# Kernel tuning notes

Hardware: AMD Instinct MI355X
Metric: run time of the kernel (lower is better)

Reference implementation:

```python
import jax, jax.numpy as jnp
import numpy as np
from jax import lax

B, T_IN, N, C_IN = 64, 12, 716, 2
RC = DC = 32      # residual / dilation channels
SC = 8            # skip channels
EC = 512          # end channels
OUT = 12
DIMS = 40
DAYS = 288
TOD = 288
TOPK = 100
DILS = [1, 2, 1, 2, 1, 2, 1, 2]  # blocks=4, layers=2
L = len(DILS)


def setup_inputs() -> dict:
    key = jax.random.key(0)
    ks = iter(jax.random.split(key, 64))
    n = lambda shape, s=0.1: jax.random.normal(next(ks), shape, jnp.float32) * s
    return dict(
        history_data=jax.random.uniform(next(ks), (B, T_IN, N, C_IN), jnp.float32),
        alpha=jnp.float32(-5.0),
        nodevec_p1=n((DAYS, DIMS), 1.0),
        nodevec_p2=n((N, DIMS), 1.0),
        nodevec_p3=n((N, DIMS), 1.0),
        nodevec_pk=n((DIMS, DIMS, DIMS), 1.0),
        pivweight=n((N, N), 1.0),
        start_W=n((RC, 1)), start_b=n((RC,)),
        starta_W=n((1, 1)), starta_b=n((1,)),
        filter_W=n((L, DC, RC, 1, 2)), filter_b=n((L, DC)),
        gate_W=n((L, DC, RC, 1, 2)), gate_b=n((L, DC)),
        skip_W=n((L, SC, DC)), skip_b=n((L, SC)),
        gconv_W=n((L, RC, 3 * DC)), gconv_b=n((L, RC)),
        pgconv_W=n((L, RC, 3 * RC)), pgconv_b=n((L, RC)),
        bn_gamma=jnp.ones((L, RC), jnp.float32),
        bn_beta=jnp.zeros((L, RC), jnp.float32),
        end1_W=n((EC, SC * 52)), end1_b=n((EC,)),
        end2_W=n((OUT, EC)), end2_b=n((OUT,)),
    )


def _conv1x1(x, W, b):  # x [B,C,N,T], W [O,C]
    return jnp.einsum('bcnt,oc->bont', x, W) + b[None, :, None, None]


def _gcn(x, A, W, b):
    # diffusion order 2 over one support; A [B,N,N] or [N,N]
    sub = 'bcvt,bwv->bcwt' if A.ndim == 3 else 'bcvt,wv->bcwt'
    x1 = jnp.einsum(sub, x, A)
    x2 = jnp.einsum(sub, x1, A)
    return _conv1x1(jnp.concatenate([x, x1, x2], axis=1), W, b)


def _forward(history_data, alpha, nodevec_p1, nodevec_p2, nodevec_p3, nodevec_pk,
             pivweight, start_W, start_b, starta_W, starta_b,
             filter_W, filter_b, gate_W, gate_b, skip_W, skip_b,
             gconv_W, gconv_b, pgconv_W, pgconv_b, bn_gamma, bn_beta,
             end1_W, end1_b, end2_W, end2_b):
    inputs = jnp.transpose(history_data[..., 0:1], (0, 3, 2, 1))  # [B,1,N,T]
    inputs = jnp.pad(inputs, ((0, 0), (0, 0), (0, 0), (1, 0)))    # T -> 13 = receptive field
    ind = (history_data[:, -1, 0, 1] * TOD).astype(jnp.int32) % DAYS

    x = _conv1x1(inputs, start_W, start_b)      # [B,RC,N,13]
    x_a = _conv1x1(inputs, starta_W, starta_b)  # [B,1,N,13]

    # dynamic adjacency (dgconstruct)
    adp = jnp.einsum('ai,ijk->ajk', nodevec_p1[ind], nodevec_pk)
    adp = jnp.einsum('bj,ajk->abk', nodevec_p2, adp)
    adp = jnp.einsum('ck,abk->abc', nodevec_p3, adp)
    adj = jax.nn.softmax(jax.nn.relu(adp), axis=2)  # [B,N,N]

    # pivotal adjacency (pivotalconstruct) with top-k node mask
    xs = x_a[:, 0].sum(0)                   # [N,T]
    y = xs.sum(1)[None, :]                  # [1,N]
    adjp = (xs[:, :-1] @ xs[:, 1:].T) / y   # [N,N]
    adjp = adjp * pivweight
    score = adjp.sum(0) + adjp.sum(1)
    _, idx = lax.top_k(score, TOPK)
    mask = jnp.zeros((N,), bool).at[idx].set(True)
    adj_p = jax.nn.softmax(jax.nn.relu(adjp * mask[:, None] * mask[None, :]), axis=1)  # [N,N]

    a_s = jax.nn.sigmoid(alpha)
    dn = ('NCHW', 'OIHW', 'NCHW')
    skip = None
    for i, d in enumerate(DILS):
        residual = x
        filt = jnp.tanh(
            lax.conv_general_dilated(residual, filter_W[i], (1, 1), 'VALID',
                                     rhs_dilation=(1, d), dimension_numbers=dn)
            + filter_b[i][None, :, None, None])
        gate = jax.nn.sigmoid(
            lax.conv_general_dilated(residual, gate_W[i], (1, 1), 'VALID',
                                     rhs_dilation=(1, d), dimension_numbers=dn)
            + gate_b[i][None, :, None, None])
        xg = _gcn(filt * gate, adj, gconv_W[i], gconv_b[i])  # [B,RC,N,T-d]
        # pgcn: diffusion on residual, then causal temporal crop by dilation
        xa = _gcn(residual, adj_p, pgconv_W[i], pgconv_b[i])[..., : residual.shape[3] - d]
        x = a_s * xa + (1.0 - a_s) * xg
        x = x + residual[..., -x.shape[3]:]
        s = _conv1x1(x, skip_W[i], skip_b[i])  # [B,SC,N,Ti]
        s = jnp.transpose(s, (0, 1, 3, 2)).reshape(s.shape[0], -1, s.shape[2], 1)  # [B,SC*Ti,N,1]
        skip = s if skip is None else jnp.concatenate([s, skip], axis=1)
        # BatchNorm2d, train-mode batch stats, fresh affine
        mu = x.mean(axis=(0, 2, 3), keepdims=True)
        var = x.var(axis=(0, 2, 3), keepdims=True)
        x = ((x - mu) / jnp.sqrt(var + 1e-5)) * bn_gamma[i][None, :, None, None] \
            + bn_beta[i][None, :, None, None]

    out = jax.nn.relu(skip)                         # [B,SC*52,N,1]
    out = jax.nn.relu(_conv1x1(out, end1_W, end1_b))
    out = _conv1x1(out, end2_W, end2_b)             # [B,OUT,N,1]
    return out


def reference(history_data, alpha, nodevec_p1, nodevec_p2, nodevec_p3, nodevec_pk,
              pivweight, start_W, start_b, starta_W, starta_b,
              filter_W, filter_b, gate_W, gate_b, skip_W, skip_b,
              gconv_W, gconv_b, pgconv_W, pgconv_b, bn_gamma, bn_beta,
              end1_W, end1_b, end2_W, end2_b):
    return _forward(history_data, alpha, nodevec_p1, nodevec_p2, nodevec_p3, nodevec_pk,
                    pivweight, start_W, start_b, starta_W, starta_b,
                    filter_W, filter_b, gate_W, gate_b, skip_W, skip_b,
                    gconv_W, gconv_b, pgconv_W, pgconv_b, bn_gamma, bn_beta,
                    end1_W, end1_b, end2_W, end2_b)
```

## Files before the change

### kernel.cpp

```cpp
#include <hip/hip_runtime.h>
#include <math.h>

#define NN 716
#define NSQ (716*716)
#define MAXG 9216
#define FPAD 70
typedef unsigned short bfu;
typedef __attribute__((ext_vector_type(8))) __bf16 bf16x8;
typedef __attribute__((ext_vector_type(4))) float f32x4;

__device__ __forceinline__ float b2f(bfu u){ union{unsigned int i; float f;} x; x.i = ((unsigned int)u)<<16; return x.f; }
__device__ __forceinline__ bfu f2b(float f){ union{float fv; unsigned int i;} x; x.fv = f; unsigned int r = (x.i + 0x7fffu + ((x.i>>16)&1u)) >> 16; return (bfu)r; }
__device__ __forceinline__ float sigmoidf_(float x){ return 1.f/(1.f+expf(-x)); }

__device__ __forceinline__ float fexp_(float x){
#if __has_builtin(__builtin_amdgcn_exp2f)
  return __builtin_amdgcn_exp2f(x * 1.44269504088896340736f);
#else
  return __expf(x);
#endif
}
__device__ __forceinline__ float frcp_(float x){
#if __has_builtin(__builtin_amdgcn_rcpf)
  return __builtin_amdgcn_rcpf(x);
#else
  return 1.f/x;
#endif
}
__device__ __forceinline__ float fsig_(float x){ return frcp_(1.f + fexp_(-x)); }
__device__ __forceinline__ float ftanh_(float x){
  float xc = fminf(fmaxf(x, -30.f), 30.f);
  float e = fexp_(-2.f*xc);
  return (1.f - e) * frcp_(1.f + e);
}


__global__ void k_ind(const float* __restrict__ hist, int* __restrict__ ind){
  int b = threadIdx.x; if (b >= 64) return;
  float v = hist[((b*12+11)*NN + 0)*2 + 1];
  ind[b] = ((int)(v*288.0f)) % 288;
}

__global__ void k_dg1(const float* __restrict__ p1, const float* __restrict__ pk,
                      const int* __restrict__ ind, float* __restrict__ tmp1){
  int b = blockIdx.x;
  __shared__ float p1s[40];
  if (threadIdx.x < 40) p1s[threadIdx.x] = p1[ind[b]*40 + threadIdx.x];
  __syncthreads();
  for (int jk = threadIdx.x; jk < 1600; jk += 256){
    float acc = 0.f;
    for (int i = 0; i < 40; ++i) acc += p1s[i]*pk[i*1600 + jk];
    tmp1[b*1600 + jk] = acc;
  }
}

__global__ void k_dg2(const float* __restrict__ p2, const float* __restrict__ tmp1,
                      float* __restrict__ tmp2){
  int b = blockIdx.y;
  __shared__ float ts[1600];
  for (int i = threadIdx.x; i < 1600; i += 256) ts[i] = tmp1[b*1600+i];
  __syncthreads();
  int idx = blockIdx.x*256 + threadIdx.x;
  if (idx >= NN*40) return;
  int n = idx/40, k = idx%40;
  float acc = 0.f;
  for (int j = 0; j < 40; ++j) acc += p2[n*40+j]*ts[j*40+k];
  tmp2[(long)b*NN*40 + idx] = acc;
}

__global__ void k_p3t(const float* __restrict__ p3, float* __restrict__ p3t){
  int v = blockIdx.x*256 + threadIdx.x; if (v >= NN) return;
  for (int k = 0; k < 40; ++k) p3t[k*NN + v] = p3[v*40 + k];
}

__global__ __launch_bounds__(256) void k_adjrow4s(const float* __restrict__ p3t,
    const float* __restrict__ tmp2, unsigned int* __restrict__ topA,
    int* __restrict__ cntA)
{
  int b = blockIdx.y, w0 = blockIdx.x*4, tid = threadIdx.x;
  int wave = tid >> 6, lane = tid & 63;
  __shared__ float t2s[4][40];
  __shared__ float buf[4][720];
  __shared__ float wred[4][4];
  __shared__ float rstat[4];
  __shared__ int pc[4][12];
  for (int i = tid; i < 160; i += 256){
    int r = i/40, k = i%40; int w = w0 + r;
    t2s[r][k] = (w < NN) ? tmp2[((long)b*NN + w)*40 + k] : 0.f;
  }
  __syncthreads();
  float lmax[4] = {0,0,0,0};
  for (int q = 0; q < 3; ++q){
    int v = tid + q*256;
    if (v < NN){
      float a[4] = {0,0,0,0};
      #pragma unroll 8
      for (int k = 0; k < 40; ++k){
        float pv = p3t[k*NN + v];
        #pragma unroll
        for (int r = 0; r < 4; ++r) a[r] += t2s[r][k]*pv;
      }
      #pragma unroll
      for (int r = 0; r < 4; ++r){
        float val = fmaxf(a[r], 0.f);
        buf[r][v] = val;
        lmax[r] = fmaxf(lmax[r], val);
      }
    }
  }
  #pragma unroll
  for (int r = 0; r < 4; ++r){
    float m = lmax[r];
    for (int s = 32; s > 0; s >>= 1) m = fmaxf(m, __shfl_xor(m, s, 64));
    if (lane == 0) wred[r][wave] = m;
  }
  __syncthreads();
  if (tid < 4) rstat[tid] = fmaxf(fmaxf(wred[tid][0], wred[tid][1]), fmaxf(wred[tid][2], wred[tid][3]));
  __syncthreads();
  float lsum[4] = {0,0,0,0};
  for (int q = 0; q < 3; ++q){
    int v = tid + q*256;
    if (v < NN){
      #pragma unroll
      for (int r = 0; r < 4; ++r){
        float e = fexp_(buf[r][v] - rstat[r]);
        buf[r][v] = e;
        lsum[r] += e;
      }
    }
  }
  __syncthreads();
  #pragma unroll
  for (int r = 0; r < 4; ++r){
    float s = lsum[r];
    for (int k = 32; k > 0; k >>= 1) s += __shfl_xor(s, k, 64);
    if (lane == 0) wred[r][wave] = s;
  }
  __syncthreads();
  if (tid < 4) rstat[tid] = frcp_(wred[tid][0] + wred[tid][1] + wred[tid][2] + wred[tid][3]);
  __syncthreads();
  for (int q = 0; q < 3; ++q){
    int v = tid + q*256;
    #pragma unroll
    for (int r = 0; r < 4; ++r){
      float p = (v < NN) ? buf[r][v]*rstat[r] : 0.f;
      unsigned long long m = __ballot(p >= 1e-7f);
      if (lane == 0) pc[r][q*4+wave] = __popcll(m);
    }
  }
  __syncthreads();
  for (int q = 0; q < 3; ++q){
    int v = tid + q*256;
    #pragma unroll
    for (int r = 0; r < 4; ++r){
      float p = (v < NN) ? buf[r][v]*rstat[r] : 0.f;
      bool qual = (p >= 1e-7f);
      unsigned long long m = __ballot(qual);
      int w = w0 + r;
      if (qual && w < NN){
        int base = 0, me = q*4+wave;
        for (int s = 0; s < me; ++s) base += pc[r][s];
        unsigned long long below = (lane == 0) ? 0ull : (m << (64-lane) >> (64-lane));
        int pos = base + __popcll(below);
        if (pos < 16)
          topA[((long)b*NN + w)*16 + pos] = (((unsigned)v)<<16) | (unsigned)f2b(p);
      }
    }
  }
  __syncthreads();
  if (tid < 4){
    int w = w0 + tid;
    if (w < NN){
      int tot = 0;
      for (int s = 0; s < 12; ++s) tot += pc[tid][s];
      cntA[(long)b*NN + w] = (tot < 16) ? tot : 16;
    }
  }
}

__global__ __launch_bounds__(256) void k_zgather2(const bfu* __restrict__ Xg,
    const unsigned int* __restrict__ topA, const int* __restrict__ cntA,
    bfu* __restrict__ Z1g, bfu* __restrict__ Z2g, int M, long sx)
{
  __shared__ bfu rows[4][720];
  __shared__ bfu zrow[4][720];
  int b = blockIdx.y;
  int tid = threadIdx.x, wave = tid >> 6, lane = tid & 63;
  int m = blockIdx.x*4 + wave;
  if (m < M){
    const bfu* xr = Xg + (long)b*sx + (long)m*NN;
    #pragma unroll
    for (int q = 0; q < 12; ++q){
      int v = lane + q*64;
      if (v < NN) rows[wave][v] = xr[v];
    }
  }
  __syncthreads();
  const unsigned int* ta = topA + (long)b*NN*16;
  const int* ca = cntA + (long)b*NN;
  if (m < M){
    bfu* zr = Z1g + (long)b*sx + (long)m*NN;
    #pragma unroll
    for (int q = 0; q < 12; ++q){
      int w = lane + q*64;
      if (w < NN){
        int cnt = ca[w];
        const unsigned int* lst = ta + (long)w*16;
        float acc = 0.f;
        for (int j = 0; j < cnt; ++j){
          unsigned int e = lst[j];
          acc += b2f((bfu)(e & 0xffffu)) * b2f(rows[wave][e >> 16]);
        }
        bfu zv = f2b(acc);
        zr[w] = zv;
        zrow[wave][w] = zv;
      }
    }
  }
  __syncthreads();
  if (m >= M) return;
  bfu* z2r = Z2g + (long)b*sx + (long)m*NN;
  #pragma unroll
  for (int q = 0; q < 12; ++q){
    int w = lane + q*64;
    if (w < NN){
      int cnt = ca[w];
      const unsigned int* lst = ta + (long)w*16;
      float acc = 0.f;
      for (int j = 0; j < cnt; ++j){
        unsigned int e = lst[j];
        acc += b2f((bfu)(e & 0xffffu)) * b2f(zrow[wave][e >> 16]);
      }
      z2r[w] = f2b(acc);
    }
  }
}

__global__ void k_xs(const float* __restrict__ hist, const float* __restrict__ saW,
                     const float* __restrict__ sab, float* __restrict__ xs, float* __restrict__ y){
  int n = blockIdx.x, b = threadIdx.x;
  float w = saW[0], bb = sab[0];
  float ytot = 0.f;
  for (int t = 0; t < 13; ++t){
    float inp = (t == 0) ? 0.f : hist[((b*12 + (t-1))*NN + n)*2];
    float s = inp;
    for (int off = 32; off > 0; off >>= 1) s += __shfl_down(s, off, 64);
    if (b == 0){ float val = w*s + 64.f*bb; xs[n*13+t] = val; ytot += val; }
  }
  if (b == 0) y[n] = ytot;
}

__global__ void k_adjp(const float* __restrict__ xs, const float* __restrict__ y,
                       const float* __restrict__ piv, float* __restrict__ adjp){
  int i = blockIdx.y;
  __shared__ float xi[13];
  if (threadIdx.x < 13) xi[threadIdx.x] = xs[i*13+threadIdx.x];
  __syncthreads();
  int j = blockIdx.x*256 + threadIdx.x;
  if (j >= NN) return;
  float acc = 0.f;
  #pragma unroll
  for (int t = 0; t < 12; ++t) acc += xi[t]*xs[j*13+t+1];
  adjp[(long)i*NN+j] = acc / y[j] * piv[(long)i*NN+j];
}

__global__ void k_score(const float* __restrict__ adjp, float* __restrict__ score){
  int n = blockIdx.x, tid = threadIdx.x;
  float s = 0.f;
  for (int i = tid; i < NN; i += 256) s += adjp[(long)i*NN+n] + adjp[(long)n*NN+i];
  __shared__ float red[256];
  red[tid] = s; __syncthreads();
  for (int k = 128; k > 0; k >>= 1){ if (tid < k) red[tid] += red[tid+k]; __syncthreads(); }
  if (tid == 0) score[n] = red[0];
}

__global__ void k_topk(const float* __restrict__ score, int* __restrict__ mask){
  __shared__ float v[1024];
  __shared__ int ix[1024];
  int tid = threadIdx.x;
  for (int t = tid; t < 1024; t += 256){ v[t] = (t < NN) ? score[t] : -INFINITY; ix[t] = t; }
  __syncthreads();
  for (int k = 2; k <= 1024; k <<= 1){
    for (int j = k >> 1; j > 0; j >>= 1){
      for (int t = tid; t < 1024; t += 256){
        int l = t ^ j;
        if (l > t){
          bool up = ((t & k) == 0);
          bool g = (v[t] > v[l]) || (v[t] == v[l] && ix[t] < ix[l]);
          if (up ? !g : g){
            float tv = v[t]; v[t] = v[l]; v[l] = tv;
            int ti = ix[t]; ix[t] = ix[l]; ix[l] = ti;
          }
        }
      }
      __syncthreads();
    }
  }
  for (int t = tid; t < NN; t += 256) mask[t] = 0;
  __syncthreads();
  if (tid < 100) mask[ix[tid]] = 1;
}

__global__ void k_pivprep(const float* __restrict__ adjp, const int* __restrict__ mask,
                          int* __restrict__ idxk, int* __restrict__ rankv,
                          float* __restrict__ uvec, float* __restrict__ ApkT){
  __shared__ int sidx[100];
  int tid = threadIdx.x;
  if (tid == 0){
    int c = 0;
    for (int i = 0; i < NN; ++i){
      if (mask[i] && c < 100){ sidx[c] = i; idxk[c] = i; rankv[i] = c; ++c; }
      else rankv[i] = -1;
    }
  }
  __syncthreads();
  if (tid < 100){
    int i = sidx[tid];
    const float* row = adjp + (long)i*NN;
    float mx = 0.f;
    for (int k = 0; k < 100; ++k) mx = fmaxf(mx, row[sidx[k]]);
    float sum = 616.f * fexp_(-mx);
    for (int k = 0; k < 100; ++k) sum += fexp_(fmaxf(row[sidx[k]], 0.f) - mx);
    float inv = 1.f/sum;
    uvec[tid] = fexp_(-mx)*inv;
    for (int k = 0; k < 100; ++k)
      ApkT[k*100 + tid] = fexp_(fmaxf(row[sidx[k]], 0.f) - mx)*inv;
  }
}

__global__ void k_init_x(const float* __restrict__ hist, const float* __restrict__ sW,
                         const float* __restrict__ sb, bfu* __restrict__ x){
  int n = blockIdx.x*256 + threadIdx.x; if (n >= NN) return;
  int t = blockIdx.y, b = blockIdx.z;
  float inp = (t == 0) ? 0.f : hist[((b*12 + (t-1))*NN + n)*2];
  #pragma unroll
  for (int c = 0; c < 32; ++c)
    x[((long)(b*32+c)*13 + t)*NN + n] = f2b(sW[c]*inp + sb[c]);
}

__global__ void k_bnid(float* __restrict__ bnp){
  int c = threadIdx.x; if (c >= 32) return;
  bnp[c*2] = 1.f; bnp[c*2+1] = 0.f;
}

__global__ void k_bnfold(const float* __restrict__ fW, const float* __restrict__ fb,
                         const float* __restrict__ gW, const float* __restrict__ gb,
                         const float* __restrict__ bnp, bfu* __restrict__ Wcat,
                         float* __restrict__ bcat){
  int tid = threadIdx.x;
  for (int i = tid; i < 4096; i += 256){
    int row = i >> 6, k = i & 63;
    int o = row >> 1, isg = row & 1;
    int tap = k >> 5, c = k & 31;
    const float* W = isg ? gW : fW;
    Wcat[i] = f2b(W[(o*32+c)*2 + tap] * bnp[c*2]);
  }
  if (tid < 64){
    int o = tid >> 1, isg = tid & 1;
    const float* W = isg ? gW : fW;
    const float* B = isg ? gb : fb;
    float s = B[o];
    for (int c = 0; c < 32; ++c)
      s += (W[(o*32+c)*2] + W[(o*32+c)*2+1]) * bnp[c*2+1];
    bcat[tid] = s;
  }
}

__global__ void k_e1perm(const float* __restrict__ W, bfu* __restrict__ Wb){
  int i = blockIdx.x*256 + threadIdx.x;
  if (i >= 512*416) return;
  int e = i/416, kp = i%416;
  const int off2[9] = {0,96,176,248,304,352,384,408,416};
  const int soff[8] = {320,240,168,112,64,32,8,0};
  const int tpl[8]  = {12,10,9,7,6,4,3,1};
  int L = 0;
  #pragma unroll
  for (int q = 0; q < 8; ++q) if (kp >= off2[q+1]) L = q+1;
  int r = kp - off2[L]; int t = r>>3, sc = r&7;
  int k = soff[L] + sc*tpl[L] + t;
  Wb[e*416+kp] = f2b(W[e*416+k]);
}

#define LDST 44

__global__ __launch_bounds__(256) void gemm_mfma(const bfu* __restrict__ Xg,
    const bfu* __restrict__ Ag, bfu* __restrict__ Cg,
    int M, int K, long sx, long sa, long sc,
    const float* __restrict__ bias, int relu_out, int Trow, int Tcomp)
{
  int bx = gridDim.x, by = gridDim.y, nb = gridDim.z;
  int bX = blockIdx.x, bY = blockIdx.y, bZ = blockIdx.z;
  int bpb = bx*by, total = bpb*nb;
  if ((total & 7) == 0 && (nb & 7) == 0){
    int L = bX + bx*(bY + by*bZ);
    int xcd = L & 7, slot = L >> 3;
    bZ = xcd*(nb >> 3) + slot/bpb;
    int inner = slot % bpb;
    bX = inner % bx; bY = inner / bx;
  }
  const bfu* X = Xg + (long)bZ*sx;
  const bfu* A = Ag + (long)bZ*sa;
  bfu*       C = Cg + (long)bZ*sc;
  int m0 = bY*128, n0 = bX*128;
  __shared__ bfu Xs[128*LDST];
  __shared__ bfu As[128*LDST];
  int tid = threadIdx.x;
  int wave = tid >> 6, lane = tid & 63;
  int wm = (wave >> 1)*64, wn = (wave & 1)*64;
  int lr = lane & 15, lg = lane >> 4;
  f32x4 acc[4][4] = {};
  int ldr = tid >> 1, ldk = (tid & 1)*16;
  int mg = m0 + ldr, ng = n0 + ldr;
  int mrow = (Trow == Tcomp) ? mg : (mg/Tcomp)*Trow + (mg%Tcomp);
  const bfu* xrow = X + (long)mrow*K;
  const bfu* arow = A + (long)ng*K;
  for (int k0 = 0; k0 < K; k0 += 32){
    int kk = k0 + ldk;
    ushort4 z4 = {0,0,0,0};
    ushort4 x0=z4,x1=z4,x2=z4,x3=z4, a0=z4,a1=z4,a2=z4,a3=z4;
    if (mg < M){
      if (kk + 16 <= K){
        const ushort4* s = (const ushort4*)(xrow + kk);
        x0=s[0]; x1=s[1]; x2=s[2]; x3=s[3];
      } else {
        bfu tv[16];
        #pragma unroll
        for (int j=0;j<16;++j) tv[j] = (kk+j < K) ? xrow[kk+j] : (bfu)0;
        const ushort4* s = (const ushort4*)tv;
        x0=s[0]; x1=s[1]; x2=s[2]; x3=s[3];
      }
    }
    if (ng < NN){
      if (kk + 16 <= K){
        const ushort4* s = (const ushort4*)(arow + kk);
        a0=s[0]; a1=s[1]; a2=s[2]; a3=s[3];
      } else {
        bfu tv[16];
        #pragma unroll
        for (int j=0;j<16;++j) tv[j] = (kk+j < K) ? arow[kk+j] : (bfu)0;
        const ushort4* s = (const ushort4*)tv;
        a0=s[0]; a1=s[1]; a2=s[2]; a3=s[3];
      }
    }
    ushort4* xd = (ushort4*)&Xs[ldr*LDST + ldk];
    xd[0]=x0; xd[1]=x1; xd[2]=x2; xd[3]=x3;
    ushort4* ad = (ushort4*)&As[ldr*LDST + ldk];
    ad[0]=a0; ad[1]=a1; ad[2]=a2; ad[3]=a3;
    __syncthreads();
    bf16x8 af[4], bfr[4];
    #pragma unroll
    for (int i=0;i<4;++i){
      af[i]  = *(const bf16x8*)&Xs[(wm + i*16 + lr)*LDST + lg*8];
      bfr[i] = *(const bf16x8*)&As[(wn + i*16 + lr)*LDST + lg*8];
    }
    #pragma unroll
    for (int i=0;i<4;++i)
      #pragma unroll
      for (int j=0;j<4;++j)
        acc[i][j] = __builtin_amdgcn_mfma_f32_16x16x32_bf16(af[i], bfr[j], acc[i][j], 0,0,0);
    __syncthreads();
  }
  #pragma unroll
  for (int i=0;i<4;++i){
    #pragma unroll
    for (int r=0;r<4;++r){
      int m = m0 + wm + i*16 + lg*4 + r;
      if (m >= M) continue;
      float bv = bias ? bias[m] : 0.f;
      #pragma unroll
      for (int j=0;j<4;++j){
        int n = n0 + wn + j*16 + lr;
        if (n < NN){
          float v = acc[i][j][r] + bv;
          if (relu_out) v = fmaxf(v, 0.f);
          C[(long)m*NN + n] = f2b(v);
        }
      }
    }
  }
}

__global__ __launch_bounds__(256) void k_fg_mfma(const bfu* __restrict__ x,
    const bfu* __restrict__ Wcat, const float* __restrict__ bcat,
    bfu* __restrict__ fg, int T, int Tp, int d)
{
  __shared__ bfu Bsh[128*FPAD];
  __shared__ bfu Ash[64*FPAD];
  __shared__ float bsh[64];
  int tid = threadIdx.x;
  int tot6 = 6*Tp;
  int L = blockIdx.x + 6*(blockIdx.y + Tp*blockIdx.z);
  int xcd = L & 7, slot = L >> 3;
  int b = xcd + ((slot/tot6) << 3);
  int r6 = slot - (slot/tot6)*tot6;
  int t = r6/6, nb6 = r6 - (r6/6)*6;
  int n0 = nb6*128;
  for (int i = tid; i < 4096; i += 256){
    int row = i >> 6, k = i & 63;
    Ash[row*FPAD + k] = Wcat[i];
  }
  if (tid < 64) bsh[tid] = bcat[tid];
  #pragma unroll
  for (int i = 0; i < 8; ++i){
    int idx = tid + i*256;
    int n4 = (idx & 31)*4;
    int cc = idx >> 5;
    int c = cc & 31, tap = cc >> 5;
    long base = ((long)(b*32+c)*T + t + (tap ? d : 0))*NN + n0 + n4;
    ushort4 v = {0,0,0,0};
    if (n0 + n4 < NN) v = *(const ushort4*)(x + base);
    Bsh[(n4+0)*FPAD + cc] = v.x;
    Bsh[(n4+1)*FPAD + cc] = v.y;
    Bsh[(n4+2)*FPAD + cc] = v.z;
    Bsh[(n4+3)*FPAD + cc] = v.w;
  }
  __syncthreads();
  int wave = tid >> 6, lane = tid & 63;
  int lr = lane & 15, lg = lane >> 4;
  int rowbase = wave*16;
  bf16x8 a0 = *(const bf16x8*)&Ash[(rowbase+lr)*FPAD + lg*8];
  bf16x8 a1 = *(const bf16x8*)&Ash[(rowbase+lr)*FPAD + 32 + lg*8];
  float bf0 = bsh[rowbase + lg*4 + 0];
  float bg0 = bsh[rowbase + lg*4 + 1];
  float bf1 = bsh[rowbase + lg*4 + 2];
  float bg1 = bsh[rowbase + lg*4 + 3];
  int o0 = (rowbase >> 1) + lg*2;
  #pragma unroll
  for (int nt = 0; nt < 8; ++nt){
    bf16x8 b0 = *(const bf16x8*)&Bsh[(nt*16+lr)*FPAD + lg*8];
    bf16x8 b1 = *(const bf16x8*)&Bsh[(nt*16+lr)*FPAD + 32 + lg*8];
    f32x4 acc = {};
    acc = __builtin_amdgcn_mfma_f32_16x16x32_bf16(a0, b0, acc, 0,0,0);
    acc = __builtin_amdgcn_mfma_f32_16x16x32_bf16(a1, b1, acc, 0,0,0);
    int n = n0 + nt*16 + lr;
    if (n < NN){
      float f0 = acc[0] + bf0, g0 = acc[1] + bg0;
      float f1 = acc[2] + bf1, g1 = acc[3] + bg1;
      fg[((long)(b*32+o0)*Tp + t)*NN + n]   = f2b(ftanh_(f0)*fsig_(g0));
      fg[((long)(b*32+o0+1)*Tp + t)*NN + n] = f2b(ftanh_(f1)*fsig_(g1));
    }
  }
}

__global__ __launch_bounds__(256) void k_pgdiff1c(const bfu* __restrict__ X,
    float* __restrict__ U, bfu* __restrict__ Yk,
    const int* __restrict__ idxk, const float* __restrict__ uvec,
    const float* __restrict__ ApkT, const float* __restrict__ bnp,
    int M, int Trow, int Tcomp)
{
  __shared__ float xks[4][100];
  int tid = threadIdx.x;
  int g = tid >> 6, lane = tid & 63;
  int m = blockIdx.x*4 + g;
  bool act = (m < M);
  float s = 0.f, sk = 0.f;
  if (act){
    int mrow = (m/Tcomp)*Trow + (m%Tcomp);
    const bfu* xr = X + (long)mrow*NN;
    #pragma unroll
    for (int q = 0; q < 12; ++q){
      int v = lane + q*64;
      if (v < NN) s += b2f(xr[v]);
    }
    for (int o = 32; o; o >>= 1) s += __shfl_xor(s, o, 64);
    #pragma unroll
    for (int q = 0; q < 2; ++q){
      int k = lane + q*64;
      if (k < 100){
        float v = b2f(xr[idxk[k]]);
        xks[g][k] = v;
        sk += v;
      }
    }
    for (int o = 32; o; o >>= 1) sk += __shfl_xor(sk, o, 64);
  }
  __syncthreads();
  if (!act) return;
  int c = (m / Tcomp) & 31;
  float sb = bnp[c*2], bb = bnp[c*2+1];
  if (lane == 0) U[m] = sb*(s*(1.f/716.f)) + bb;
  #pragma unroll
  for (int q = 0; q < 2; ++q){
    int r = lane + q*64;
    if (r < 100){
      float acc = uvec[r]*(s - sk);
      for (int k = 0; k < 100; ++k) acc += ApkT[k*100 + r]*xks[g][k];
      Yk[(long)m*100 + r] = f2b(sb*acc + bb);
    }
  }
}

__global__ __launch_bounds__(256) void k_pgdiff2c(const float* __restrict__ U1,
    const bfu* __restrict__ Y1k, float* __restrict__ U2, bfu* __restrict__ Y2k,
    const float* __restrict__ uvec, const float* __restrict__ ApkT, int M)
{
  __shared__ float yks[4][100];
  int tid = threadIdx.x;
  int g = tid >> 6, lane = tid & 63;
  int m = blockIdx.x*4 + g;
  bool act = (m < M);
  float sumY = 0.f;
  if (act){
    const bfu* yr = Y1k + (long)m*100;
    #pragma unroll
    for (int q = 0; q < 2; ++q){
      int k = lane + q*64;
      if (k < 100){
        float v = b2f(yr[k]);
        yks[g][k] = v;
        sumY += v;
      }
    }
    for (int o = 32; o; o >>= 1) sumY += __shfl_xor(sumY, o, 64);
  }
  __syncthreads();
  if (!act) return;
  float base = 616.f*U1[m];
  if (lane == 0) U2[m] = (base + sumY)*(1.f/716.f);
  #pragma unroll
  for (int q = 0; q < 2; ++q){
    int r = lane + q*64;
    if (r < 100){
      float acc = uvec[r]*base;
      for (int k = 0; k < 100; ++k) acc += ApkT[k*100 + r]*yks[g][k];
      Y2k[(long)m*100 + r] = f2b(acc);
    }
  }
}

__global__ __launch_bounds__(256) void k_ymix(const float* __restrict__ U1,
    const float* __restrict__ U2, const bfu* __restrict__ Y1k, const bfu* __restrict__ Y2k,
    const float* __restrict__ pWl, float* __restrict__ V12, float* __restrict__ M12, int Tp)
{
  int t = blockIdx.x, b = blockIdx.y, tid = threadIdx.x;
  __shared__ float w1t[1024], w2t[1024];
  __shared__ float y1s[3200], y2s[3200];
  __shared__ float u1s[32], u2s[32];
  for (int i = tid; i < 1024; i += 256){
    int o = i & 31, c = i >> 5;
    w1t[c*32+o] = pWl[o*96+32+c];
    w2t[c*32+o] = pWl[o*96+64+c];
  }
  for (int i = tid; i < 3200; i += 256){
    int c = i/100, r = i - c*100;
    long m = (long)(b*32+c)*Tp + t;
    y1s[i] = b2f(Y1k[m*100 + r]);
    y2s[i] = b2f(Y2k[m*100 + r]);
  }
  if (tid < 32){
    long m = (long)(b*32+tid)*Tp + t;
    u1s[tid] = U1[m]; u2s[tid] = U2[m];
  }
  __syncthreads();
  for (int i = tid; i < 3200; i += 256){
    int r = i >> 5, o = i & 31;
    float acc = 0.f;
    #pragma unroll 8
    for (int c = 0; c < 32; ++c)
      acc += w1t[c*32+o]*y1s[c*100+r] + w2t[c*32+o]*y2s[c*100+r];
    M12[((long)(b*Tp+t)*100 + r)*32 + o] = acc;
  }
  if (tid < 32){
    float acc = 0.f;
    #pragma unroll 8
    for (int c = 0; c < 32; ++c)
      acc += w1t[c*32+tid]*u1s[c] + w2t[c*32+tid]*u2s[c];
    V12[(long)(b*Tp+t)*32 + tid] = acc;
  }
}


__global__ __launch_bounds__(256) void k_xgmix1n(bfu* __restrict__ F,
    const bfu* __restrict__ z1, const bfu* __restrict__ z2,
    const float* __restrict__ Wl, const float* __restrict__ bl,
    const float* __restrict__ alpha, int Tp)
{
  __shared__ float w0t[1024], w1t[1024], w2t[1024], bb[32];
  for (int i = threadIdx.x; i < 1024; i += 256){
    int o = i & 31, c = i >> 5;
    w0t[c*32+o] = Wl[o*96+c];
    w1t[c*32+o] = Wl[o*96+32+c];
    w2t[c*32+o] = Wl[o*96+64+c];
  }
  if (threadIdx.x < 32) bb[threadIdx.x] = bl[threadIdx.x];
  __syncthreads();
  int n = blockIdx.x*256 + threadIdx.x; if (n >= NN) return;
  int t = blockIdx.y, b = blockIdx.z;
  float acc[32];
  #pragma unroll
  for (int o = 0; o < 32; ++o) acc[o] = bb[o];
  const float4* w04 = (const float4*)w0t;
  const float4* w14 = (const float4*)w1t;
  const float4* w24 = (const float4*)w2t;
  #pragma unroll 4
  for (int c = 0; c < 32; ++c){
    long off = ((long)(b*32+c)*Tp + t)*NN + n;
    float f0 = b2f(F[off]);
    float a0 = b2f(z1[off]);
    float b0 = b2f(z2[off]);
    #pragma unroll
    for (int o4 = 0; o4 < 8; ++o4){
      float4 w0v = w04[c*8+o4], w1v = w14[c*8+o4], w2v = w24[c*8+o4];
      acc[o4*4+0] += w0v.x*f0 + w1v.x*a0 + w2v.x*b0;
      acc[o4*4+1] += w0v.y*f0 + w1v.y*a0 + w2v.y*b0;
      acc[o4*4+2] += w0v.z*f0 + w1v.z*a0 + w2v.z*b0;
      acc[o4*4+3] += w0v.w*f0 + w1v.w*a0 + w2v.w*b0;
    }
  }
  float oma = 1.f - sigmoidf_(alpha[0]);
  #pragma unroll
  for (int o = 0; o < 32; ++o)
    F[((long)(b*32+o)*Tp + t)*NN + n] = f2b(oma*acc[o]);
}

__global__ __launch_bounds__(256) void k_combine3nc(const bfu* __restrict__ x,
    bfu* __restrict__ F, const int* __restrict__ rankv,
    const float* __restrict__ M12, const float* __restrict__ V12,
    const float* __restrict__ pWl, const float* __restrict__ pbl,
    const float* __restrict__ skWl, const float* __restrict__ skbl,
    const float* __restrict__ alpha, const float* __restrict__ bnp,
    bfu* __restrict__ skipP, float* __restrict__ bnred,
    int T, int Tp, int d, int off2)
{
  __shared__ float w0t[1024];
  __shared__ bfu Msb[101*34];
  __shared__ float swt[256], bnl[64], pbs[32], sb8[8];
  int tid = threadIdx.x;
  int tot2 = 2*Tp;
  int L = blockIdx.x + 2*(blockIdx.y + Tp*blockIdx.z);
  int xcd = L & 7, slot = L >> 3;
  int b = xcd + ((slot/tot2) << 3);
  int r2 = slot - (slot/tot2)*tot2;
  int t = r2/2, bx2 = r2 & 1;
  for (int i = tid; i < 1024; i += 256){
    int o = i & 31, c = i >> 5;
    w0t[c*32+o] = pWl[o*96+c];
  }
  for (int i = tid; i < 3434; i += 256){
    int r = i/34, o = i - r*34;
    if (o < 32)
      Msb[r*34+o] = f2b((r < 100) ? M12[((long)(b*Tp+t)*100 + r)*32 + o]
                                  : V12[(long)(b*Tp+t)*32 + o]);
  }
  swt[tid] = skWl[tid];
  if (tid < 64) bnl[tid] = bnp[tid];
  if (tid < 32) pbs[tid] = pbl[tid];
  if (tid < 8)  sb8[tid] = skbl[tid];
  __syncthreads();
  int n = bx2*512 + tid*2;
  bool act = (n < NN);
  float ax[32], ay[32];
  #pragma unroll
  for (int o = 0; o < 32; ++o){ ax[o] = pbs[o]; ay[o] = pbs[o]; }
  const float4* w04 = (const float4*)w0t;
  if (act){
    #pragma unroll 2
    for (int c = 0; c < 32; ++c){
      float sc = bnl[c*2], bc = bnl[c*2+1];
      ushort2 xv = *(const ushort2*)(x + ((long)(b*32+c)*T + t)*NN + n);
      float x0 = b2f(xv.x)*sc + bc;
      float x1 = b2f(xv.y)*sc + bc;
      #pragma unroll
      for (int o4 = 0; o4 < 8; ++o4){
        float4 w = w04[c*8+o4];
        ax[o4*4+0] += w.x*x0;  ay[o4*4+0] += w.x*x1;
        ax[o4*4+1] += w.y*x0;  ay[o4*4+1] += w.y*x1;
        ax[o4*4+2] += w.z*x0;  ay[o4*4+2] += w.z*x1;
        ax[o4*4+3] += w.w*x0;  ay[o4*4+3] += w.w*x1;
      }
    }
  }
  int ra = act ? rankv[n]   : -1;
  int rb = act ? rankv[n+1] : -1;
  int sela = (ra < 0) ? 100 : ra;
  int selb = (rb < 0) ? 100 : rb;
  float a_s = sigmoidf_(alpha[0]);
  #pragma unroll
  for (int o = 0; o < 32; ++o){
    float v0 = 0.f, v1 = 0.f;
    if (act){
      float scb = bnl[o*2], bcb = bnl[o*2+1];
      long oidx = ((long)(b*32+o)*Tp + t)*NN + n;
      ushort2 gv = *(const ushort2*)(F + oidx);
      ushort2 rv = *(const ushort2*)(x + ((long)(b*32+o)*T + t + d)*NN + n);
      v0 = a_s*(ax[o] + b2f(Msb[sela*34+o])) + b2f(gv.x) + b2f(rv.x)*scb + bcb;
      v1 = a_s*(ay[o] + b2f(Msb[selb*34+o])) + b2f(gv.y) + b2f(rv.y)*scb + bcb;
      ushort2 ov; ov.x = f2b(v0); ov.y = f2b(v1);
      *(ushort2*)(F + oidx) = ov;
    }
    ax[o] = v0; ay[o] = v1;
  }
  {
    int wave = tid >> 6;
    int gid = ((blockIdx.x + gridDim.x*(blockIdx.y + gridDim.y*blockIdx.z)) << 2) + wave;
    #pragma unroll
    for (int o = 0; o < 32; ++o){
      float v  = ax[o] + ay[o];
      float vq = ax[o]*ax[o] + ay[o]*ay[o];
      for (int s = 32; s; s >>= 1){
        v  += __shfl_xor(v,  s, 64);
        vq += __shfl_xor(vq, s, 64);
      }
      if ((tid & 63) == 0){
        bnred[((long)o*MAXG + gid)*2]     = v;
        bnred[((long)o*MAXG + gid)*2 + 1] = vq;
      }
    }
  }
  if (!act) return;
  const float4* sw4 = (const float4*)swt;
  #pragma unroll
  for (int sc2 = 0; sc2 < 8; ++sc2){
    float s0 = sb8[sc2], s1 = sb8[sc2];
    #pragma unroll
    for (int c4 = 0; c4 < 8; ++c4){
      float4 w = sw4[sc2*8 + c4];
      s0 += w.x*ax[c4*4] + w.y*ax[c4*4+1] + w.z*ax[c4*4+2] + w.w*ax[c4*4+3];
      s1 += w.x*ay[c4*4] + w.y*ay[c4*4+1] + w.z*ay[c4*4+2] + w.w*ay[c4*4+3];
    }
    ushort2 ov; ov.x = f2b(fmaxf(s0, 0.f)); ov.y = f2b(fmaxf(s1, 0.f));
    *(ushort2*)(skipP + ((long)b*416 + off2 + t*8 + sc2)*NN + n) = ov;
  }
}

__global__ void k_bn2v2(const float* __restrict__ red, const float* __restrict__ gamma,
                        const float* __restrict__ beta, float* __restrict__ bnp,
                        int layer, int Tp, int ngroups){
  int c = blockIdx.x, tid = threadIdx.x;
  float s = 0.f, s2 = 0.f;
  for (int g = tid; g < ngroups; g += 256){
    s  += red[((long)c*MAXG + g)*2];
    s2 += red[((long)c*MAXG + g)*2 + 1];
  }
  __shared__ float rs[256], rs2[256];
  rs[tid] = s; rs2[tid] = s2; __syncthreads();
  for (int k = 128; k > 0; k >>= 1){
    if (tid < k){ rs[tid] += rs[tid+k]; rs2[tid] += rs2[tid+k]; }
    __syncthreads();
  }
  if (tid == 0){
    float cnt = 64.f*Tp*716.f;
    float mu = rs[0]/cnt, var = rs2[0]/cnt - mu*mu;
    float rstd = rsqrtf(var + 1e-5f);
    float ga = gamma[layer*32+c], be = beta[layer*32+c];
    bnp[c*2] = rstd*ga; bnp[c*2+1] = be - mu*rstd*ga;
  }
}


__global__ __launch_bounds__(256) void k_sktr(const bfu* __restrict__ SP, bfu* __restrict__ ST){
  __shared__ bfu tile[64][66];
  int b = blockIdx.z;
  int n0 = blockIdx.x*64, k0 = blockIdx.y*64;
  int tid = threadIdx.x;
  int tr = tid >> 6, tc = tid & 63;
  #pragma unroll
  for (int p = 0; p < 16; ++p){
    int k = k0 + p*4 + tr, n = n0 + tc;
    tile[p*4+tr][tc] = (k < 416 && n < NN) ? SP[((long)b*416 + k)*NN + n] : (bfu)0;
  }
  __syncthreads();
  #pragma unroll
  for (int p = 0; p < 16; ++p){
    int n = n0 + p*4 + tr, k = k0 + tc;
    if (n < NN && k < 416) ST[((long)b*NN + n)*416 + k] = tile[tc][p*4+tr];
  }
}

__global__ __launch_bounds__(256) void k_end2(const bfu* __restrict__ H,
    const float* __restrict__ W2, const float* __restrict__ b2, float* __restrict__ out)
{
  __shared__ float w[12*512];
  for (int i = threadIdx.x; i < 6144; i += 256) w[i] = W2[i];
  __syncthreads();
  int n = blockIdx.x*256 + threadIdx.x; if (n >= NN) return;
  int b = blockIdx.y;
  float acc[12];
  #pragma unroll
  for (int o = 0; o < 12; ++o) acc[o] = b2[o];
  for (int e = 0; e < 512; ++e){
    float h = b2f(H[((long)b*512+e)*NN + n]);
    #pragma unroll
    for (int o = 0; o < 12; ++o) acc[o] += w[o*512+e]*h;
  }
  #pragma unroll
  for (int o = 0; o < 12; ++o) out[((long)b*12+o)*NN + n] = acc[o];
}


extern "C" void kernel_launch(void* const* d_in, const int* in_sizes, int n_in,
                              void* d_out, int out_size, void* d_ws, size_t ws_size,
                              hipStream_t stream)
{
  const float* hist = (const float*)d_in[0];
  const float* alpha = (const float*)d_in[1];
  const float* p1  = (const float*)d_in[2];
  const float* p2  = (const float*)d_in[3];
  const float* p3  = (const float*)d_in[4];
  const float* pk  = (const float*)d_in[5];
  const float* piv = (const float*)d_in[6];
  const float* sW  = (const float*)d_in[7];
  const float* sb  = (const float*)d_in[8];
  const float* saW = (const float*)d_in[9];
  const float* sab = (const float*)d_in[10];
  const float* fW  = (const float*)d_in[11];
  const float* fb  = (const float*)d_in[12];
  const float* gW  = (const float*)d_in[13];
  const float* gb  = (const float*)d_in[14];
  const float* skW = (const float*)d_in[15];
  const float* skb = (const float*)d_in[16];
  const float* gcW = (const float*)d_in[17];
  const float* gcb = (const float*)d_in[18];
  const float* pgW = (const float*)d_in[19];
  const float* pgb = (const float*)d_in[20];
  const float* bng = (const float*)d_in[21];
  const float* bnb = (const float*)d_in[22];
  const float* e1W = (const float*)d_in[23];
  const float* e1b = (const float*)d_in[24];
  const float* e2W = (const float*)d_in[25];
  const float* e2b = (const float*)d_in[26];
  float* out = (float*)d_out;

  char* base = (char*)d_ws;
  size_t off = 0;
  auto alloc = [&](size_t bytes)->char*{
    char* r = base + off;
    off = (off + bytes + 255) & ~(size_t)255;
    return r;
  };
  const size_t SZ12 = 64UL*32*12*716*2;
  const size_t SZ13 = 64UL*32*13*716*2;
  bfu*   t1    = (bfu*)  alloc(SZ12);
  bfu*   t2    = (bfu*)  alloc(SZ12);
  bfu*   P     = (bfu*)  alloc(SZ13);
  bfu*   Q     = (bfu*)  alloc(SZ12);
  bfu*   skipP = (bfu*)  alloc(64UL*416*716*2);
  bfu*   skipT = (bfu*)  alloc(64UL*716*416*2);
  float* adjp  = (float*)alloc((size_t)NSQ*4);
  float* tmp1  = (float*)alloc(64UL*1600*4);
  float* tmp2  = (float*)alloc(64UL*716*40*4);
  float* p3t   = (float*)alloc(40UL*716*4);
  bfu*   e1Wb  = (bfu*)  alloc(512UL*416*2);
  unsigned int* topA = (unsigned int*)alloc(64UL*NN*16*4);
  int*   cntA  = (int*)  alloc(64UL*NN*4);
  bfu*   Wcat  = (bfu*)  alloc(4096UL*2);
  float* bcat  = (float*)alloc(64UL*4);
  float* xs    = (float*)alloc(716UL*13*4);
  float* yv    = (float*)alloc(716UL*4);
  float* score = (float*)alloc(716UL*4);
  float* bnred = (float*)alloc(32UL*MAXG*2*4);
  float* bnp   = (float*)alloc(64UL*4);
  float* bnpid = (float*)alloc(64UL*4);
  float* uvec  = (float*)alloc(100UL*4);
  float* ApkT  = (float*)alloc(100UL*100*4);
  int*   ind   = (int*)  alloc(64UL*4);
  int*   mask  = (int*)  alloc(716UL*4);
  int*   idxk  = (int*)  alloc(100UL*4);
  int*   rankv = (int*)  alloc(716UL*4);

  char* t1c = (char*)t1;
  float* U1  = (float*)(t1c);
  float* U2  = (float*)(t1c +   98304);
  float* V12 = (float*)(t1c + 2*98304);
  float* M12 = (float*)(t1c + 3*98304);
  bfu*   Y1k = (bfu*)  (t1c + 3*98304 + 9830400);
  bfu*   Y2k = (bfu*)  (t1c + 3*98304 + 9830400 + 4915200);

  bfu* hidden = t1;

  k_ind<<<1,64,0,stream>>>(hist, ind);
  k_dg1<<<64,256,0,stream>>>(p1, pk, ind, tmp1);
  k_dg2<<<dim3(112,64),256,0,stream>>>(p2, tmp1, tmp2);
  k_p3t<<<3,256,0,stream>>>(p3, p3t);
  k_adjrow4s<<<dim3(179,64),256,0,stream>>>(p3t, tmp2, topA, cntA);
  k_xs<<<716,64,0,stream>>>(hist, saW, sab, xs, yv);
  k_adjp<<<dim3(3,716),256,0,stream>>>(xs, yv, piv, adjp);
  k_score<<<716,256,0,stream>>>(adjp, score);
  k_topk<<<1,256,0,stream>>>(score, mask);
  k_pivprep<<<1,256,0,stream>>>(adjp, mask, idxk, rankv, uvec, ApkT);
  k_init_x<<<dim3(3,13,64),256,0,stream>>>(hist, sW, sb, P);
  k_e1perm<<<(512*416+255)/256,256,0,stream>>>(e1W, e1Wb);
  k_bnid<<<1,64,0,stream>>>(bnpid);

  int T = 13;
  bfu* x = P;
  bfu* F = Q;
  static const int off2_[8] = {0,96,176,248,304,352,384,408};
  for (int i = 0; i < 8; ++i){
    int d = (i & 1) ? 2 : 1;
    int Tp = T - d;
    const float* bnin = (i == 0) ? bnpid : bnp;
    dim3 g3(3, Tp, 64);
    dim3 g2n(2, Tp, 64);
    k_bnfold<<<1,256,0,stream>>>(fW + i*2048, fb + i*32, gW + i*2048, gb + i*32,
        bnin, Wcat, bcat);
    k_fg_mfma<<<dim3(6,Tp,64),256,0,stream>>>(x, Wcat, bcat, F, T, Tp, d);
    int M1 = 32*Tp; long sx1 = (long)M1*NN;
    dim3 gz((M1+3)/4, 64);
    k_zgather2<<<gz,256,0,stream>>>(F, topA, cntA, t1, t2, M1, sx1);
    k_xgmix1n<<<g3,256,0,stream>>>(F, t1, t2, gcW + i*3072, gcb + i*32, alpha, Tp);
    int M2 = 64*32*Tp;
    k_pgdiff1c<<<M2/4,256,0,stream>>>(x, U1, Y1k, idxk, uvec, ApkT, bnin, M2, T, Tp);
    k_pgdiff2c<<<M2/4,256,0,stream>>>(U1, Y1k, U2, Y2k, uvec, ApkT, M2);
    k_ymix<<<dim3(Tp,64),256,0,stream>>>(U1, U2, Y1k, Y2k, pgW + i*3072, V12, M12, Tp);
    k_combine3nc<<<g2n,256,0,stream>>>(x, F, rankv, M12, V12, pgW + i*3072, pgb + i*32,
        skW + i*256, skb + i*8, alpha, bnin, skipP, bnred, T, Tp, d, off2_[i]);
    int ngroups = 2*Tp*64*4;
    k_bn2v2<<<32,256,0,stream>>>(bnred, bng, bnb, bnp, i, Tp, ngroups);
    bfu* tmp = x; x = F; F = tmp;
    T = Tp;
  }
  k_sktr<<<dim3(12,7,64),256,0,stream>>>(skipP, skipT);
  gemm_mfma<<<dim3(6,4,64),256,0,stream>>>(e1Wb, skipT, hidden, 512, 416,
      0L, 416L*716, 512L*716, e1b, 1, 1, 1);
  k_end2<<<dim3(3,64),256,0,stream>>>(hidden, e2W, e2b, out);
}
```

Baseline: 2.754 ms.

## Use MFMA for graph-conv channel mix, fuse BN weight folding and pivot diffusion kernels

Replaces the scalar FP32 per-node 96->32 channel-mix kernel with an MFMA bf16 kernel that stages the F/z1/z2 tiles in LDS. BN folding of the filter/gate weights moves inside the fg MFMA kernel, which removes a separate single-block launch per layer. The two pivot diffusion kernels are merged into one so Y1 stays in shared memory instead of being re-read from global. The bf16 MFMA path lowers the precision of the mixing step, and every fg block now repeats the small weight-folding work.

New measurement: 2.545 ms. 7.6% less time.

```diff
diff --git a/kernel.cpp b/kernel.cpp
--- a/kernel.cpp
+++ b/kernel.cpp
@@ -5,6 +5,7 @@
 #define NSQ (716*716)
 #define MAXG 9216
 #define FPAD 70
+#define XPAD 102
 typedef unsigned short bfu;
 typedef __attribute__((ext_vector_type(8))) __bf16 bf16x8;
 typedef __attribute__((ext_vector_type(4))) float f32x4;
@@ -341,29 +342,6 @@
 __global__ void k_bnid(float* __restrict__ bnp){
   int c = threadIdx.x; if (c >= 32) return;
   bnp[c*2] = 1.f; bnp[c*2+1] = 0.f;
-}
-
-__global__ void k_bnfold(const float* __restrict__ fW, const float* __restrict__ fb,
-                         const float* __restrict__ gW, const float* __restrict__ gb,
-                         const float* __restrict__ bnp, bfu* __restrict__ Wcat,
-                         float* __restrict__ bcat){
-  int tid = threadIdx.x;
-  for (int i = tid; i < 4096; i += 256){
-    int row = i >> 6, k = i & 63;
-    int o = row >> 1, isg = row & 1;
-    int tap = k >> 5, c = k & 31;
-    const float* W = isg ? gW : fW;
-    Wcat[i] = f2b(W[(o*32+c)*2 + tap] * bnp[c*2]);
-  }
-  if (tid < 64){
-    int o = tid >> 1, isg = tid & 1;
-    const float* W = isg ? gW : fW;
-    const float* B = isg ? gb : fb;
-    float s = B[o];
-    for (int c = 0; c < 32; ++c)
-      s += (W[(o*32+c)*2] + W[(o*32+c)*2+1]) * bnp[c*2+1];
-    bcat[tid] = s;
-  }
 }
 
 __global__ void k_e1perm(const float* __restrict__ W, bfu* __restrict__ Wb){
@@ -481,8 +459,9 @@
 }
 
 __global__ __launch_bounds__(256) void k_fg_mfma(const bfu* __restrict__ x,
-    const bfu* __restrict__ Wcat, const float* __restrict__ bcat,
-    bfu* __restrict__ fg, int T, int Tp, int d)
+    const float* __restrict__ fWl, const float* __restrict__ fbl,
+    const float* __restrict__ gWl, const float* __restrict__ gbl,
+    const float* __restrict__ bnp, bfu* __restrict__ fg, int T, int Tp, int d)
 {
   __shared__ bfu Bsh[128*FPAD];
   __shared__ bfu Ash[64*FPAD];
@@ -497,9 +476,20 @@
   int n0 = nb6*128;
   for (int i = tid; i < 4096; i += 256){
     int row = i >> 6, k = i & 63;
-    Ash[row*FPAD + k] = Wcat[i];
-  }
-  if (tid < 64) bsh[tid] = bcat[tid];
+    int o = row >> 1, isg = row & 1;
+    int tap = k >> 5, c = k & 31;
+    const float* W = isg ? gWl : fWl;
+    Ash[row*FPAD + k] = f2b(W[(o*32+c)*2 + tap] * bnp[c*2]);
+  }
+  if (tid < 64){
+    int o = tid >> 1, isg = tid & 1;
+    const float* W = isg ? gWl : fWl;
+    const float* B = isg ? gbl : fbl;
+    float s = B[o];
+    for (int c = 0; c < 32; ++c)
+      s += (W[(o*32+c)*2] + W[(o*32+c)*2+1]) * bnp[c*2+1];
+    bsh[tid] = s;
+  }
   #pragma unroll
   for (int i = 0; i < 8; ++i){
     int idx = tid + i*256;
@@ -542,13 +532,81 @@
   }
 }
 
-__global__ __launch_bounds__(256) void k_pgdiff1c(const bfu* __restrict__ X,
-    float* __restrict__ U, bfu* __restrict__ Yk,
+__global__ __launch_bounds__(256) void k_xgmix_mfma(bfu* __restrict__ F,
+    const bfu* __restrict__ z1, const bfu* __restrict__ z2,
+    const float* __restrict__ Wl, const float* __restrict__ bl,
+    const float* __restrict__ alpha, int Tp)
+{
+  __shared__ bfu Bsh[128*XPAD];
+  __shared__ bfu Ash[32*XPAD];
+  __shared__ float bsh[32];
+  int tid = threadIdx.x;
+  int tot6 = 6*Tp;
+  int L = blockIdx.x + 6*(blockIdx.y + Tp*blockIdx.z);
+  int xcd = L & 7, slot = L >> 3;
+  int b = xcd + ((slot/tot6) << 3);
+  int r6 = slot - (slot/tot6)*tot6;
+  int t = r6/6, nb6 = r6 - (r6/6)*6;
+  int n0 = nb6*128;
+  for (int i = tid; i < 3072; i += 256){
+    int o = i/96, k = i - o*96;
+    Ash[o*XPAD + k] = f2b(Wl[i]);
+  }
+  if (tid < 32) bsh[tid] = bl[tid];
+  #pragma unroll
+  for (int i = 0; i < 12; ++i){
+    int idx = tid + i*256;
+    int cc = idx % 96;
+    int n4 = (idx / 96) * 4;
+    const bfu* src = (cc < 32) ? F : ((cc < 64) ? z1 : z2);
+    int c = cc & 31;
+    long base = ((long)(b*32+c)*Tp + t)*NN + n0 + n4;
+    ushort4 v = {0,0,0,0};
+    if (n0 + n4 < NN) v = *(const ushort4*)(src + base);
+    Bsh[(n4+0)*XPAD + cc] = v.x;
+    Bsh[(n4+1)*XPAD + cc] = v.y;
+    Bsh[(n4+2)*XPAD + cc] = v.z;
+    Bsh[(n4+3)*XPAD + cc] = v.w;
+  }
+  __syncthreads();
+  int wave = tid >> 6, lane = tid & 63;
+  int lr = lane & 15, lg = lane >> 4;
+  int rt = wave & 1;
+  int ntb = wave >> 1;
+  bf16x8 a0 = *(const bf16x8*)&Ash[(rt*16+lr)*XPAD + 0  + lg*8];
+  bf16x8 a1 = *(const bf16x8*)&Ash[(rt*16+lr)*XPAD + 32 + lg*8];
+  bf16x8 a2 = *(const bf16x8*)&Ash[(rt*16+lr)*XPAD + 64 + lg*8];
+  float oma = 1.f - sigmoidf_(alpha[0]);
+  #pragma unroll
+  for (int j = 0; j < 4; ++j){
+    int nt = ntb + j*2;
+    bf16x8 b0 = *(const bf16x8*)&Bsh[(nt*16+lr)*XPAD + 0  + lg*8];
+    bf16x8 b1 = *(const bf16x8*)&Bsh[(nt*16+lr)*XPAD + 32 + lg*8];
+    bf16x8 b2 = *(const bf16x8*)&Bsh[(nt*16+lr)*XPAD + 64 + lg*8];
+    f32x4 acc = {};
+    acc = __builtin_amdgcn_mfma_f32_16x16x32_bf16(a0, b0, acc, 0,0,0);
+    acc = __builtin_amdgcn_mfma_f32_16x16x32_bf16(a1, b1, acc, 0,0,0);
+    acc = __builtin_amdgcn_mfma_f32_16x16x32_bf16(a2, b2, acc, 0,0,0);
+    int n = n0 + nt*16 + lr;
+    if (n < NN){
+      #pragma unroll
+      for (int r = 0; r < 4; ++r){
+        int o = rt*16 + lg*4 + r;
+        F[((long)(b*32+o)*Tp + t)*NN + n] = f2b(oma*(acc[r] + bsh[o]));
+      }
+    }
+  }
+}
+
+__global__ __launch_bounds__(256) void k_pgdiff12(const bfu* __restrict__ X,
+    float* __restrict__ U1, bfu* __restrict__ Y1k,
+    float* __restrict__ U2, bfu* __restrict__ Y2k,
     const int* __restrict__ idxk, const float* __restrict__ uvec,
     const float* __restrict__ ApkT, const float* __restrict__ bnp,
     int M, int Trow, int Tcomp)
 {
   __shared__ float xks[4][100];
+  __shared__ float yks[4][100];
   int tid = threadIdx.x;
   int g = tid >> 6, lane = tid & 63;
   int m = blockIdx.x*4 + g;
@@ -575,47 +633,30 @@
     for (int o = 32; o; o >>= 1) sk += __shfl_xor(sk, o, 64);
   }
   __syncthreads();
+  float u1val = 0.f, sumY = 0.f;
+  if (act){
+    int c = (m / Tcomp) & 31;
+    float sb = bnp[c*2], bb = bnp[c*2+1];
+    u1val = sb*(s*(1.f/716.f)) + bb;
+    if (lane == 0) U1[m] = u1val;
+    #pragma unroll
+    for (int q = 0; q < 2; ++q){
+      int r = lane + q*64;
+      if (r < 100){
+        float acc = uvec[r]*(s - sk);
+        for (int k = 0; k < 100; ++k) acc += ApkT[k*100 + r]*xks[g][k];
+        bfu yv = f2b(sb*acc + bb);
+        Y1k[(long)m*100 + r] = yv;
+        float yf = b2f(yv);
+        yks[g][r] = yf;
+        sumY += yf;
+      }
+    }
+    for (int o = 32; o; o >>= 1) sumY += __shfl_xor(sumY, o, 64);
+  }
+  __syncthreads();
   if (!act) return;
-  int c = (m / Tcomp) & 31;
-  float sb = bnp[c*2], bb = bnp[c*2+1];
-  if (lane == 0) U[m] = sb*(s*(1.f/716.f)) + bb;
-  #pragma unroll
-  for (int q = 0; q < 2; ++q){
-    int r = lane + q*64;
-    if (r < 100){
-      float acc = uvec[r]*(s - sk);
-      for (int k = 0; k < 100; ++k) acc += ApkT[k*100 + r]*xks[g][k];
-      Yk[(long)m*100 + r] = f2b(sb*acc + bb);
-    }
-  }
-}
-
-__global__ __launch_bounds__(256) void k_pgdiff2c(const float* __restrict__ U1,
-    const bfu* __restrict__ Y1k, float* __restrict__ U2, bfu* __restrict__ Y2k,
-    const float* __restrict__ uvec, const float* __restrict__ ApkT, int M)
-{
-  __shared__ float yks[4][100];
-  int tid = threadIdx.x;
-  int g = tid >> 6, lane = tid & 63;
-  int m = blockIdx.x*4 + g;
-  bool act = (m < M);
-  float sumY = 0.f;
-  if (act){
-    const bfu* yr = Y1k + (long)m*100;
-    #pragma unroll
-    for (int q = 0; q < 2; ++q){
-      int k = lane + q*64;
-      if (k < 100){
-        float v = b2f(yr[k]);
-        yks[g][k] = v;
-        sumY += v;
-      }
-    }
-    for (int o = 32; o; o >>= 1) sumY += __shfl_xor(sumY, o, 64);
-  }
-  __syncthreads();
-  if (!act) return;
-  float base = 616.f*U1[m];
+  float base = 616.f*u1val;
   if (lane == 0) U2[m] = (base + sumY)*(1.f/716.f);
   #pragma unroll
   for (int q = 0; q < 2; ++q){
@@ -667,50 +708,6 @@
       acc += w1t[c*32+tid]*u1s[c] + w2t[c*32+tid]*u2s[c];
     V12[(long)(b*Tp+t)*32 + tid] = acc;
   }
-}
-
-
-__global__ __launch_bounds__(256) void k_xgmix1n(bfu* __restrict__ F,
-    const bfu* __restrict__ z1, const bfu* __restrict__ z2,
-    const float* __restrict__ Wl, const float* __restrict__ bl,
-    const float* __restrict__ alpha, int Tp)
-{
-  __shared__ float w0t[1024], w1t[1024], w2t[1024], bb[32];
-  for (int i = threadIdx.x; i < 1024; i += 256){
-    int o = i & 31, c = i >> 5;
-    w0t[c*32+o] = Wl[o*96+c];
-    w1t[c*32+o] = Wl[o*96+32+c];
-    w2t[c*32+o] = Wl[o*96+64+c];
-  }
-  if (threadIdx.x < 32) bb[threadIdx.x] = bl[threadIdx.x];
-  __syncthreads();
-  int n = blockIdx.x*256 + threadIdx.x; if (n >= NN) return;
-  int t = blockIdx.y, b = blockIdx.z;
-  float acc[32];
-  #pragma unroll
-  for (int o = 0; o < 32; ++o) acc[o] = bb[o];
-  const float4* w04 = (const float4*)w0t;
-  const float4* w14 = (const float4*)w1t;
-  const float4* w24 = (const float4*)w2t;
-  #pragma unroll 4
-  for (int c = 0; c < 32; ++c){
-    long off = ((long)(b*32+c)*Tp + t)*NN + n;
-    float f0 = b2f(F[off]);
-    float a0 = b2f(z1[off]);
-    float b0 = b2f(z2[off]);
-    #pragma unroll
-    for (int o4 = 0; o4 < 8; ++o4){
-      float4 w0v = w04[c*8+o4], w1v = w14[c*8+o4], w2v = w24[c*8+o4];
-      acc[o4*4+0] += w0v.x*f0 + w1v.x*a0 + w2v.x*b0;
-      acc[o4*4+1] += w0v.y*f0 + w1v.y*a0 + w2v.y*b0;
-      acc[o4*4+2] += w0v.z*f0 + w1v.z*a0 + w2v.z*b0;
-      acc[o4*4+3] += w0v.w*f0 + w1v.w*a0 + w2v.w*b0;
-    }
-  }
-  float oma = 1.f - sigmoidf_(alpha[0]);
-  #pragma unroll
-  for (int o = 0; o < 32; ++o)
-    F[((long)(b*32+o)*Tp + t)*NN + n] = f2b(oma*acc[o]);
 }
 
 __global__ __launch_bounds__(256) void k_combine3nc(const bfu* __restrict__ x,
@@ -943,8 +940,6 @@
   bfu*   e1Wb  = (bfu*)  alloc(512UL*416*2);
   unsigned int* topA = (unsigned int*)alloc(64UL*NN*16*4);
   int*   cntA  = (int*)  alloc(64UL*NN*4);
-  bfu*   Wcat  = (bfu*)  alloc(4096UL*2);
-  float* bcat  = (float*)alloc(64UL*4);
   float* xs    = (float*)alloc(716UL*13*4);
   float* yv    = (float*)alloc(716UL*4);
   float* score = (float*)alloc(716UL*4);
@@ -990,18 +985,17 @@
     int d = (i & 1) ? 2 : 1;
     int Tp = T - d;
     const float* bnin = (i == 0) ? bnpid : bnp;
-    dim3 g3(3, Tp, 64);
     dim3 g2n(2, Tp, 64);
-    k_bnfold<<<1,256,0,stream>>>(fW + i*2048, fb + i*32, gW + i*2048, gb + i*32,
-        bnin, Wcat, bcat);
-    k_fg_mfma<<<dim3(6,Tp,64),256,0,stream>>>(x, Wcat, bcat, F, T, Tp, d);
+    dim3 g6(6, Tp, 64);
+    k_fg_mfma<<<g6,256,0,stream>>>(x, fW + i*2048, fb + i*32, gW + i*2048, gb + i*32,
+        bnin, F, T, Tp, d);
     int M1 = 32*Tp; long sx1 = (long)M1*NN;
     dim3 gz((M1+3)/4, 64);
     k_zgather2<<<gz,256,0,stream>>>(F, topA, cntA, t1, t2, M1, sx1);
-    k_xgmix1n<<<g3,256,0,stream>>>(F, t1, t2, gcW + i*3072, gcb + i*32, alpha, Tp);
+    k_xgmix_mfma<<<g6,256,0,stream>>>(F, t1, t2, gcW + i*3072, gcb + i*32, alpha, Tp);
     int M2 = 64*32*Tp;
-    k_pgdiff1c<<<M2/4,256,0,stream>>>(x, U1, Y1k, idxk, uvec, ApkT, bnin, M2, T, Tp);
-    k_pgdiff2c<<<M2/4,256,0,stream>>>(U1, Y1k, U2, Y2k, uvec, ApkT, M2);
+    k_pgdiff12<<<M2/4,256,0,stream>>>(x, U1, Y1k, U2, Y2k, idxk, uvec, ApkT, bnin,
+        M2, T, Tp);
     k_ymix<<<dim3(Tp,64),256,0,stream>>>(U1, U2, Y1k, Y2k, pgW + i*3072, V12, M12, Tp);
     k_combine3nc<<<g2n,256,0,stream>>>(x, F, rankv, M12, V12, pgW + i*3072, pgb + i*32,
         skW + i*256, skb + i*8, alpha, bnin, skipP, bnred, T, Tp, d, off2_[i]);
```
